# Kernel optimization log

Measured on AMD Instinct MI355X. Metric: run time of the kernel, lower is better.

Reference implementation:

```python
import jax, jax.numpy as jnp
import numpy as np

N = 131072
D = 64
K = 1024
COMMITMENT_COST = 0.25


def setup_inputs() -> dict:
    key = jax.random.key(0)
    k1, k2 = jax.random.split(key)
    inputs = jax.random.normal(k1, (N, D), dtype=jnp.float32)
    # nn.Embedding weight initialized uniform(-1/K, 1/K)
    codebook = jax.random.uniform(k2, (K, D), dtype=jnp.float32,
                                  minval=-1.0 / K, maxval=1.0 / K)
    return {"inputs": inputs, "codebook": codebook}


def reference(inputs, codebook):
    # distances[n,k] = ||x_n||^2 + ||e_k||^2 - 2 x_n . e_k   (squared L2)
    distances = (jnp.sum(inputs ** 2, axis=1, keepdims=True)
                 + jnp.sum(codebook ** 2, axis=1)
                 - 2.0 * jnp.matmul(inputs, codebook.T))          # [N, K]
    encoding_indices = jnp.argmin(distances, axis=1)               # [N]
    # one-hot scatter + matmul in the original == direct gather
    quantized = codebook[encoding_indices]                         # [N, D]

    e_latent_loss = jnp.mean((jax.lax.stop_gradient(quantized) - inputs) ** 2)
    q_latent_loss = jnp.mean((quantized - jax.lax.stop_gradient(inputs)) ** 2)
    loss = q_latent_loss + COMMITMENT_COST * e_latent_loss

    # straight-through estimator
    quantized_st = inputs + jax.lax.stop_gradient(quantized - inputs)
    return loss, quantized_st, encoding_indices
```

## Files before the change

### kernel.cpp

```cpp
#include <hip/hip_runtime.h>

#define NN 131072
#define DD 64
#define KK 1024

typedef __attribute__((ext_vector_type(8))) short short8v;
typedef __attribute__((ext_vector_type(4))) float float4v;
typedef __attribute__((ext_vector_type(4))) int int4v;

#define MFMA(a, b, c) __builtin_amdgcn_mfma_f32_16x16x32_bf16(a, b, c, 0, 0, 0)

#define INS3(t0, t1, t2, i0, i1, i2, u, kk)                                  \
    if ((u) < (t0)) { t2 = t1; i2 = i1; t1 = t0; i1 = i0; t0 = (u); i0 = (kk); } \
    else if ((u) < (t1)) { t2 = t1; i2 = i1; t1 = (u); i1 = (kk); }          \
    else if ((u) < (t2)) { t2 = (u); i2 = (kk); }

#define LEXINS3(t0, t1, t2, i0, i1, i2, u, kk)                               \
    if ((u) < (t0) || ((u) == (t0) && (kk) < (i0))) {                        \
        t2 = t1; i2 = i1; t1 = t0; i1 = i0; t0 = (u); i0 = (kk); }           \
    else if ((u) < (t1) || ((u) == (t1) && (kk) < (i1))) {                   \
        t2 = t1; i2 = i1; t1 = (u); i1 = (kk); }                             \
    else if ((u) < (t2) || ((u) == (t2) && (kk) < (i2))) { t2 = (u); i2 = (kk); }

__device__ __forceinline__ float np_sumsq64(const float* v) {
    float r[8];
#pragma unroll
    for (int j = 0; j < 8; ++j) r[j] = __fmul_rn(v[j], v[j]);
#pragma unroll
    for (int i = 8; i < 64; i += 8) {
#pragma unroll
        for (int j = 0; j < 8; ++j)
            r[j] = __fadd_rn(r[j], __fmul_rn(v[i + j], v[i + j]));
    }
    return __fadd_rn(__fadd_rn(__fadd_rn(r[0], r[1]), __fadd_rn(r[2], r[3])),
                     __fadd_rn(__fadd_rn(r[4], r[5]), __fadd_rn(r[6], r[7])));
}

__device__ __forceinline__ void bf16split(float v, unsigned short& hb, unsigned short& lb) {
    unsigned int u = __builtin_bit_cast(unsigned int, v);
    unsigned int h = (u + 0x7FFFu + ((u >> 16) & 1u)) >> 16;
    float hf = __builtin_bit_cast(float, h << 16);
    float lo = __fsub_rn(v, hf);
    unsigned int ul = __builtin_bit_cast(unsigned int, lo);
    unsigned int lo16 = (ul + 0x7FFFu + ((ul >> 16) & 1u)) >> 16;
    hb = (unsigned short)h;
    lb = (unsigned short)lo16;
}

__global__ void vq_prep(const float* __restrict__ cb, unsigned short* __restrict__ cbh,
                        unsigned short* __restrict__ cbl, float* __restrict__ se) {
    int k = blockIdx.x * 256 + threadIdx.x;
    if (k >= KK) return;
    float v[DD];
    const float4* p = (const float4*)(cb + (size_t)k * DD);
#pragma unroll
    for (int i = 0; i < 16; ++i) {
        float4 q = p[i];
        v[4 * i + 0] = q.x; v[4 * i + 1] = q.y; v[4 * i + 2] = q.z; v[4 * i + 3] = q.w;
    }
    se[k] = np_sumsq64(v);
    short8v* oh = (short8v*)(cbh + (size_t)k * DD);
    short8v* ol = (short8v*)(cbl + (size_t)k * DD);
#pragma unroll
    for (int q = 0; q < 8; ++q) {
        short8v hq, lq;
#pragma unroll
        for (int e = 0; e < 8; ++e) {
            unsigned short hb, lb;
            bf16split(v[q * 8 + e], hb, lb);
            hq[e] = (short)hb; lq[e] = (short)lb;
        }
        oh[q] = hq; ol[q] = lq;
    }
}

__global__ __launch_bounds__(256)
void vq_main(const float* __restrict__ x, const float* __restrict__ cb,
             const unsigned short* __restrict__ cbh, const unsigned short* __restrict__ cbl,
             const float* __restrict__ se, float* __restrict__ qout,
             float* __restrict__ idxf, double* __restrict__ acc) {
    __shared__ unsigned short xh[128 * 64], xl[128 * 64];
    __shared__ unsigned short ebh[128 * 64], ebl[128 * 64];
    __shared__ float ses[KK];
    __shared__ float wls[4];

    const int tid = threadIdx.x;
    const int rowBase = blockIdx.x * 128;
    const int l = tid & 63;
    const int w = tid >> 6;
    const int col = l & 15;
    const int g = l >> 4;

    ((float4v*)ses)[tid] = ((const float4v*)se)[tid];

    {
        int row = tid >> 1, db = (tid & 1) * 32;
        const float* xr = x + (size_t)(rowBase + row) * 64 + db;
#pragma unroll
        for (int jj = 0; jj < 4; ++jj) {
            float4 v0 = ((const float4*)xr)[2 * jj];
            float4 v1 = ((const float4*)xr)[2 * jj + 1];
            float vv[8] = {v0.x, v0.y, v0.z, v0.w, v1.x, v1.y, v1.z, v1.w};
            short8v hq, lq;
#pragma unroll
            for (int e = 0; e < 8; ++e) {
                unsigned short hb, lb;
                bf16split(vv[e], hb, lb);
                hq[e] = (short)hb; lq[e] = (short)lb;
            }
            int q = (tid & 1) * 4 + jj;
            int slot = row * 8 + (q ^ (row & 7));
            ((short8v*)xh)[slot] = hq;
            ((short8v*)xl)[slot] = lq;
        }
    }
    __syncthreads();

    short8v ah0s0, ah1s0, al0s0, al1s0, ah0s1, ah1s1, al0s1, al1s1;
    {
        int r0 = w * 32 + col;
        int r1 = r0 + 16;
        ah0s0 = ((short8v*)xh)[r0 * 8 + ((0 + g) ^ (r0 & 7))];
        ah1s0 = ((short8v*)xh)[r0 * 8 + ((4 + g) ^ (r0 & 7))];
        al0s0 = ((short8v*)xl)[r0 * 8 + ((0 + g) ^ (r0 & 7))];
        al1s0 = ((short8v*)xl)[r0 * 8 + ((4 + g) ^ (r0 & 7))];
        ah0s1 = ((short8v*)xh)[r1 * 8 + ((0 + g) ^ (r1 & 7))];
        ah1s1 = ((short8v*)xh)[r1 * 8 + ((4 + g) ^ (r1 & 7))];
        al0s1 = ((short8v*)xl)[r1 * 8 + ((0 + g) ^ (r1 & 7))];
        al1s1 = ((short8v*)xl)[r1 * 8 + ((4 + g) ^ (r1 & 7))];
    }

    float bt[8][3];
    int bix[8][3];
#pragma unroll
    for (int s = 0; s < 8; ++s) {
#pragma unroll
        for (int j = 0; j < 3; ++j) { bt[s][j] = 3.4e38f; bix[s][j] = 0x7FFFFFF; }
    }

    int4v rbh[4], rbl[4];
    {
        int e = tid >> 1;
        const unsigned short* ph = cbh + (size_t)e * 64 + (tid & 1) * 32;
        const unsigned short* pl = cbl + (size_t)e * 64 + (tid & 1) * 32;
#pragma unroll
        for (int jj = 0; jj < 4; ++jj) {
            rbh[jj] = *(const int4v*)(ph + jj * 8);
            rbl[jj] = *(const int4v*)(pl + jj * 8);
        }
    }

    for (int t = 0; t < 8; ++t) {
        __syncthreads();
        {
            int e = tid >> 1;
#pragma unroll
            for (int jj = 0; jj < 4; ++jj) {
                int q = (tid & 1) * 4 + jj;
                int slot = e * 8 + (q ^ (e & 7));
                ((int4v*)ebh)[slot] = rbh[jj];
                ((int4v*)ebl)[slot] = rbl[jj];
            }
        }
        __syncthreads();
        if (t < 7) {
            int e = tid >> 1;
            const unsigned short* ph = cbh + (size_t)((t + 1) * 128 + e) * 64 + (tid & 1) * 32;
            const unsigned short* pl = cbl + (size_t)((t + 1) * 128 + e) * 64 + (tid & 1) * 32;
#pragma unroll
            for (int jj = 0; jj < 4; ++jj) {
                rbh[jj] = *(const int4v*)(ph + jj * 8);
                rbl[jj] = *(const int4v*)(pl + jj * 8);
            }
        }

#pragma unroll
        for (int c = 0; c < 8; ++c) {
            int ec = c * 16 + col;
            int be = ec * 8, sw = ec & 7;
            short8v bh0 = ((short8v*)ebh)[be + ((0 + g) ^ sw)];
            short8v bh1 = ((short8v*)ebh)[be + ((4 + g) ^ sw)];
            short8v bl0 = ((short8v*)ebl)[be + ((0 + g) ^ sw)];
            short8v bl1 = ((short8v*)ebl)[be + ((4 + g) ^ sw)];
            float sek = ses[t * 128 + ec];
            float4v acc0 = {0.f, 0.f, 0.f, 0.f}, acc1 = {0.f, 0.f, 0.f, 0.f};
            acc0 = MFMA(ah0s0, bh0, acc0);
            acc0 = MFMA(ah1s0, bh1, acc0);
            acc0 = MFMA(al0s0, bh0, acc0);
            acc0 = MFMA(al1s0, bh1, acc0);
            acc0 = MFMA(ah0s0, bl0, acc0);
            acc0 = MFMA(ah1s0, bl1, acc0);
            acc1 = MFMA(ah0s1, bh0, acc1);
            acc1 = MFMA(ah1s1, bh1, acc1);
            acc1 = MFMA(al0s1, bh0, acc1);
            acc1 = MFMA(al1s1, bh1, acc1);
            acc1 = MFMA(ah0s1, bl0, acc1);
            acc1 = MFMA(ah1s1, bl1, acc1);
            int kk = t * 128 + ec;
#pragma unroll
            for (int r = 0; r < 4; ++r) {
                float u0 = fmaf(-2.f, acc0[r], sek);
                INS3(bt[r][0], bt[r][1], bt[r][2], bix[r][0], bix[r][1], bix[r][2], u0, kk);
                float u1 = fmaf(-2.f, acc1[r], sek);
                INS3(bt[4 + r][0], bt[4 + r][1], bt[4 + r][2],
                     bix[4 + r][0], bix[4 + r][1], bix[4 + r][2], u1, kk);
            }
        }
    }

#pragma unroll
    for (int s = 0; s < 8; ++s) {
#pragma unroll
        for (int m = 1; m < 16; m <<= 1) {
            float o0 = __shfl_xor(bt[s][0], m), o1 = __shfl_xor(bt[s][1], m), o2 = __shfl_xor(bt[s][2], m);
            int q0 = __shfl_xor(bix[s][0], m), q1 = __shfl_xor(bix[s][1], m), q2 = __shfl_xor(bix[s][2], m);
            LEXINS3(bt[s][0], bt[s][1], bt[s][2], bix[s][0], bix[s][1], bix[s][2], o0, q0);
            LEXINS3(bt[s][0], bt[s][1], bt[s][2], bix[s][0], bix[s][1], bix[s][2], o1, q1);
            LEXINS3(bt[s][0], bt[s][1], bt[s][2], bix[s][0], bix[s][1], bix[s][2], o2, q2);
        }
    }

    float lossLocal = 0.f;
    const int rr = (l & 15) >> 2;
    const int j = l & 3;
    const int jj = (j == 3) ? 0 : j;
#pragma unroll
    for (int s = 0; s < 2; ++s) {
        int ck = bix[s * 4][0];
#pragma unroll
        for (int r_ = 0; r_ < 4; ++r_) {
#pragma unroll
            for (int j_ = 0; j_ < 3; ++j_) {
                if (rr == r_ && jj == j_) ck = bix[s * 4 + r_][j_];
            }
        }
        int rowg = rowBase + w * 32 + s * 16 + g * 4 + rr;
        const float4* xr = (const float4*)(x + (size_t)rowg * 64);
        const float4* er = (const float4*)(cb + (size_t)ck * 64);
        float dot = 0.f;
        float rs0 = 0.f, rs1 = 0.f, rs2 = 0.f, rs3 = 0.f, rs4 = 0.f, rs5 = 0.f, rs6 = 0.f, rs7 = 0.f;
#pragma unroll
        for (int i = 0; i < 16; ++i) {
            float4 a4 = xr[i], e4 = er[i];
            dot = fmaf(a4.x, e4.x, dot);
            dot = fmaf(a4.y, e4.y, dot);
            dot = fmaf(a4.z, e4.z, dot);
            dot = fmaf(a4.w, e4.w, dot);
            if ((i & 1) == 0) {
                rs0 = __fadd_rn(rs0, __fmul_rn(a4.x, a4.x));
                rs1 = __fadd_rn(rs1, __fmul_rn(a4.y, a4.y));
                rs2 = __fadd_rn(rs2, __fmul_rn(a4.z, a4.z));
                rs3 = __fadd_rn(rs3, __fmul_rn(a4.w, a4.w));
            } else {
                rs4 = __fadd_rn(rs4, __fmul_rn(a4.x, a4.x));
                rs5 = __fadd_rn(rs5, __fmul_rn(a4.y, a4.y));
                rs6 = __fadd_rn(rs6, __fmul_rn(a4.z, a4.z));
                rs7 = __fadd_rn(rs7, __fmul_rn(a4.w, a4.w));
            }
        }
        float sa = __fadd_rn(__fadd_rn(__fadd_rn(rs0, rs1), __fadd_rn(rs2, rs3)),
                             __fadd_rn(__fadd_rn(rs4, rs5), __fadd_rn(rs6, rs7)));
        float qd = __fsub_rn(__fadd_rn(sa, ses[ck]), __fmul_rn(2.f, dot));
#pragma unroll
        for (int m = 1; m < 4; m <<= 1) {
            float oq = __shfl_xor(qd, m);
            int ok = __shfl_xor(ck, m);
            if (oq < qd || (oq == qd && ok < ck)) { qd = oq; ck = ok; }
        }
        if (j == 0) idxf[rowg] = (float)ck;
        const float4* qr = (const float4*)(cb + (size_t)ck * 64);
        float* orow = qout + (size_t)rowg * 64;
#pragma unroll
        for (int p = 0; p < 4; ++p) {
            int iq = j * 4 + p;
            float4 xv = xr[iq];
            float4 qv = qr[iq];
            float dx = __fsub_rn(qv.x, xv.x);
            float dy = __fsub_rn(qv.y, xv.y);
            float dz = __fsub_rn(qv.z, xv.z);
            float dw = __fsub_rn(qv.w, xv.w);
            float4 o;
            o.x = __fadd_rn(xv.x, dx);
            o.y = __fadd_rn(xv.y, dy);
            o.z = __fadd_rn(xv.z, dz);
            o.w = __fadd_rn(xv.w, dw);
            ((float4*)orow)[iq] = o;
            lossLocal = fmaf(dx, dx, lossLocal);
            lossLocal = fmaf(dy, dy, lossLocal);
            lossLocal = fmaf(dz, dz, lossLocal);
            lossLocal = fmaf(dw, dw, lossLocal);
        }
    }
#pragma unroll
    for (int m = 1; m < 64; m <<= 1) lossLocal += __shfl_xor(lossLocal, m);
    if (l == 0) wls[w] = lossLocal;
    __syncthreads();
    if (tid == 0) atomicAdd(acc, (double)(wls[0] + wls[1] + wls[2] + wls[3]));
}

__global__ void vq_loss(const double* __restrict__ acc, float* __restrict__ out) {
    out[0] = (float)(acc[0] * 1.25 / (double)((size_t)NN * DD));
}

extern "C" void kernel_launch(void* const* d_in, const int* in_sizes, int n_in,
                              void* d_out, int out_size, void* d_ws, size_t ws_size,
                              hipStream_t stream) {
    const float* x = (const float*)d_in[0];
    const float* cb = (const float*)d_in[1];
    float* out = (float*)d_out;

    double* acc = (double*)d_ws;
    float* se = (float*)((char*)d_ws + 64);
    unsigned short* cbh = (unsigned short*)((char*)d_ws + 8192);
    unsigned short* cbl = (unsigned short*)((char*)d_ws + 8192 + 131072);

    hipMemsetAsync(d_ws, 0, 64, stream);

    vq_prep<<<4, 256, 0, stream>>>(cb, cbh, cbl, se);
    vq_main<<<NN / 128, 256, 0, stream>>>(x, cb, cbh, cbl, se,
                                          out + 1, out + 1 + (size_t)NN * DD, acc);
    vq_loss<<<1, 1, 0, stream>>>(acc, out);
}
```

Measured before the change: 237.7 us.

## Pack distance and index into sortable keys, double-buffer smaller codebook tiles

Result: faster. 195.4 us (-17.8%).

```diff
diff --git a/kernel.cpp b/kernel.cpp
--- a/kernel.cpp
+++ b/kernel.cpp
@@ -10,17 +10,19 @@
 
 #define MFMA(a, b, c) __builtin_amdgcn_mfma_f32_16x16x32_bf16(a, b, c, 0, 0, 0)
 
-#define INS3(t0, t1, t2, i0, i1, i2, u, kk)                                  \
-    if ((u) < (t0)) { t2 = t1; i2 = i1; t1 = t0; i1 = i0; t0 = (u); i0 = (kk); } \
-    else if ((u) < (t1)) { t2 = t1; i2 = i1; t1 = (u); i1 = (kk); }          \
-    else if ((u) < (t2)) { t2 = (u); i2 = (kk); }
-
-#define LEXINS3(t0, t1, t2, i0, i1, i2, u, kk)                               \
-    if ((u) < (t0) || ((u) == (t0) && (kk) < (i0))) {                        \
-        t2 = t1; i2 = i1; t1 = t0; i1 = i0; t0 = (u); i0 = (kk); }           \
-    else if ((u) < (t1) || ((u) == (t1) && (kk) < (i1))) {                   \
-        t2 = t1; i2 = i1; t1 = (u); i1 = (kk); }                             \
-    else if ((u) < (t2) || ((u) == (t2) && (kk) < (i2))) { t2 = (u); i2 = (kk); }
+__device__ __forceinline__ unsigned int umin32(unsigned int a, unsigned int b) { return a < b ? a : b; }
+__device__ __forceinline__ unsigned int umax32(unsigned int a, unsigned int b) { return a > b ? a : b; }
+
+__device__ __forceinline__ unsigned int packu(float u, int kk) {
+    int b = __builtin_bit_cast(int, u);
+    unsigned int key = (unsigned int)(b ^ ((b >> 31) | 0x80000000));
+    return (key & 0xFFFFFC00u) | (unsigned int)kk;
+}
+
+#define PINS3(t0, t1, t2, p)                                   \
+    { unsigned int _x0 = umax32(t0, p); t0 = umin32(t0, p);    \
+      unsigned int _x1 = umax32(t1, _x0); t1 = umin32(t1, _x0);\
+      t2 = umin32(t2, _x1); }
 
 __device__ __forceinline__ float np_sumsq64(const float* v) {
     float r[8];
@@ -74,13 +76,17 @@
     }
 }
 
-__global__ __launch_bounds__(256)
+union SMem {
+    struct { unsigned short xh[128 * 64]; unsigned short xl[128 * 64]; } x;
+    struct { unsigned short bh[2][64 * 64]; unsigned short bl[2][64 * 64]; } b;
+};
+
+__global__ __launch_bounds__(256, 4)
 void vq_main(const float* __restrict__ x, const float* __restrict__ cb,
              const unsigned short* __restrict__ cbh, const unsigned short* __restrict__ cbl,
              const float* __restrict__ se, float* __restrict__ qout,
              float* __restrict__ idxf, double* __restrict__ acc) {
-    __shared__ unsigned short xh[128 * 64], xl[128 * 64];
-    __shared__ unsigned short ebh[128 * 64], ebl[128 * 64];
+    __shared__ SMem sm;
     __shared__ float ses[KK];
     __shared__ float wls[4];
 
@@ -90,6 +96,21 @@
     const int w = tid >> 6;
     const int col = l & 15;
     const int g = l >> 4;
+
+    int4v rbh[2], rbl[2];
+    const int be_ = tid >> 2;
+    const int bq_ = (tid & 3) * 2;
+#define LOAD_TILE(tt)                                                              \
+    { const unsigned short* ph = cbh + ((size_t)((tt) * 64 + be_) * 64) + (tid & 3) * 16; \
+      const unsigned short* pl = cbl + ((size_t)((tt) * 64 + be_) * 64) + (tid & 3) * 16; \
+      rbh[0] = *(const int4v*)(ph); rbh[1] = *(const int4v*)(ph + 8);              \
+      rbl[0] = *(const int4v*)(pl); rbl[1] = *(const int4v*)(pl + 8); }
+#define WRITE_TILE(bufi)                                                           \
+    { int4v* dh = (int4v*)sm.b.bh[bufi]; int4v* dl = (int4v*)sm.b.bl[bufi];        \
+      dh[be_ * 8 + (bq_ ^ (be_ & 7))] = rbh[0];                                    \
+      dh[be_ * 8 + ((bq_ + 1) ^ (be_ & 7))] = rbh[1];                              \
+      dl[be_ * 8 + (bq_ ^ (be_ & 7))] = rbl[0];                                    \
+      dl[be_ * 8 + ((bq_ + 1) ^ (be_ & 7))] = rbl[1]; }
 
     ((float4v*)ses)[tid] = ((const float4v*)se)[tid];
 
@@ -110,79 +131,52 @@
             }
             int q = (tid & 1) * 4 + jj;
             int slot = row * 8 + (q ^ (row & 7));
-            ((short8v*)xh)[slot] = hq;
-            ((short8v*)xl)[slot] = lq;
-        }
-    }
+            ((short8v*)sm.x.xh)[slot] = hq;
+            ((short8v*)sm.x.xl)[slot] = lq;
+        }
+    }
+    LOAD_TILE(0);
     __syncthreads();
 
     short8v ah0s0, ah1s0, al0s0, al1s0, ah0s1, ah1s1, al0s1, al1s1;
     {
         int r0 = w * 32 + col;
         int r1 = r0 + 16;
-        ah0s0 = ((short8v*)xh)[r0 * 8 + ((0 + g) ^ (r0 & 7))];
-        ah1s0 = ((short8v*)xh)[r0 * 8 + ((4 + g) ^ (r0 & 7))];
-        al0s0 = ((short8v*)xl)[r0 * 8 + ((0 + g) ^ (r0 & 7))];
-        al1s0 = ((short8v*)xl)[r0 * 8 + ((4 + g) ^ (r0 & 7))];
-        ah0s1 = ((short8v*)xh)[r1 * 8 + ((0 + g) ^ (r1 & 7))];
-        ah1s1 = ((short8v*)xh)[r1 * 8 + ((4 + g) ^ (r1 & 7))];
-        al0s1 = ((short8v*)xl)[r1 * 8 + ((0 + g) ^ (r1 & 7))];
-        al1s1 = ((short8v*)xl)[r1 * 8 + ((4 + g) ^ (r1 & 7))];
-    }
-
-    float bt[8][3];
-    int bix[8][3];
-#pragma unroll
-    for (int s = 0; s < 8; ++s) {
-#pragma unroll
-        for (int j = 0; j < 3; ++j) { bt[s][j] = 3.4e38f; bix[s][j] = 0x7FFFFFF; }
-    }
-
-    int4v rbh[4], rbl[4];
-    {
-        int e = tid >> 1;
-        const unsigned short* ph = cbh + (size_t)e * 64 + (tid & 1) * 32;
-        const unsigned short* pl = cbl + (size_t)e * 64 + (tid & 1) * 32;
-#pragma unroll
-        for (int jj = 0; jj < 4; ++jj) {
-            rbh[jj] = *(const int4v*)(ph + jj * 8);
-            rbl[jj] = *(const int4v*)(pl + jj * 8);
-        }
-    }
-
-    for (int t = 0; t < 8; ++t) {
-        __syncthreads();
-        {
-            int e = tid >> 1;
-#pragma unroll
-            for (int jj = 0; jj < 4; ++jj) {
-                int q = (tid & 1) * 4 + jj;
-                int slot = e * 8 + (q ^ (e & 7));
-                ((int4v*)ebh)[slot] = rbh[jj];
-                ((int4v*)ebl)[slot] = rbl[jj];
-            }
-        }
-        __syncthreads();
-        if (t < 7) {
-            int e = tid >> 1;
-            const unsigned short* ph = cbh + (size_t)((t + 1) * 128 + e) * 64 + (tid & 1) * 32;
-            const unsigned short* pl = cbl + (size_t)((t + 1) * 128 + e) * 64 + (tid & 1) * 32;
-#pragma unroll
-            for (int jj = 0; jj < 4; ++jj) {
-                rbh[jj] = *(const int4v*)(ph + jj * 8);
-                rbl[jj] = *(const int4v*)(pl + jj * 8);
-            }
-        }
-
-#pragma unroll
-        for (int c = 0; c < 8; ++c) {
+        ah0s0 = ((short8v*)sm.x.xh)[r0 * 8 + ((0 + g) ^ (r0 & 7))];
+        ah1s0 = ((short8v*)sm.x.xh)[r0 * 8 + ((4 + g) ^ (r0 & 7))];
+        al0s0 = ((short8v*)sm.x.xl)[r0 * 8 + ((0 + g) ^ (r0 & 7))];
+        al1s0 = ((short8v*)sm.x.xl)[r0 * 8 + ((4 + g) ^ (r0 & 7))];
+        ah0s1 = ((short8v*)sm.x.xh)[r1 * 8 + ((0 + g) ^ (r1 & 7))];
+        ah1s1 = ((short8v*)sm.x.xh)[r1 * 8 + ((4 + g) ^ (r1 & 7))];
+        al0s1 = ((short8v*)sm.x.xl)[r1 * 8 + ((0 + g) ^ (r1 & 7))];
+        al1s1 = ((short8v*)sm.x.xl)[r1 * 8 + ((4 + g) ^ (r1 & 7))];
+    }
+    __syncthreads();
+
+    WRITE_TILE(0);
+    LOAD_TILE(1);
+    __syncthreads();
+
+    unsigned int k0[8], k1[8], k2[8];
+#pragma unroll
+    for (int s = 0; s < 8; ++s) { k0[s] = 0xFFFFFFFFu; k1[s] = 0xFFFFFFFFu; k2[s] = 0xFFFFFFFFu; }
+
+    for (int t = 0; t < 16; ++t) {
+        if (t < 15) {
+            WRITE_TILE((t + 1) & 1);
+            if (t < 14) LOAD_TILE(t + 2);
+        }
+        const unsigned short* bhB = sm.b.bh[t & 1];
+        const unsigned short* blB = sm.b.bl[t & 1];
+#pragma unroll
+        for (int c = 0; c < 4; ++c) {
             int ec = c * 16 + col;
             int be = ec * 8, sw = ec & 7;
-            short8v bh0 = ((short8v*)ebh)[be + ((0 + g) ^ sw)];
-            short8v bh1 = ((short8v*)ebh)[be + ((4 + g) ^ sw)];
-            short8v bl0 = ((short8v*)ebl)[be + ((0 + g) ^ sw)];
-            short8v bl1 = ((short8v*)ebl)[be + ((4 + g) ^ sw)];
-            float sek = ses[t * 128 + ec];
+            short8v bh0 = ((const short8v*)bhB)[be + ((0 + g) ^ sw)];
+            short8v bh1 = ((const short8v*)bhB)[be + ((4 + g) ^ sw)];
+            short8v bl0 = ((const short8v*)blB)[be + ((0 + g) ^ sw)];
+            short8v bl1 = ((const short8v*)blB)[be + ((4 + g) ^ sw)];
+            float sek = ses[t * 64 + ec];
             float4v acc0 = {0.f, 0.f, 0.f, 0.f}, acc1 = {0.f, 0.f, 0.f, 0.f};
             acc0 = MFMA(ah0s0, bh0, acc0);
             acc0 = MFMA(ah1s0, bh1, acc0);
@@ -196,27 +190,29 @@
             acc1 = MFMA(al1s1, bh1, acc1);
             acc1 = MFMA(ah0s1, bl0, acc1);
             acc1 = MFMA(ah1s1, bl1, acc1);
-            int kk = t * 128 + ec;
+            int kk = t * 64 + ec;
 #pragma unroll
             for (int r = 0; r < 4; ++r) {
-                float u0 = fmaf(-2.f, acc0[r], sek);
-                INS3(bt[r][0], bt[r][1], bt[r][2], bix[r][0], bix[r][1], bix[r][2], u0, kk);
-                float u1 = fmaf(-2.f, acc1[r], sek);
-                INS3(bt[4 + r][0], bt[4 + r][1], bt[4 + r][2],
-                     bix[4 + r][0], bix[4 + r][1], bix[4 + r][2], u1, kk);
+                unsigned int p0 = packu(fmaf(-2.f, acc0[r], sek), kk);
+                PINS3(k0[r], k1[r], k2[r], p0);
+                unsigned int p1 = packu(fmaf(-2.f, acc1[r], sek), kk);
+                PINS3(k0[4 + r], k1[4 + r], k2[4 + r], p1);
             }
         }
+        __syncthreads();
     }
 
 #pragma unroll
     for (int s = 0; s < 8; ++s) {
 #pragma unroll
         for (int m = 1; m < 16; m <<= 1) {
-            float o0 = __shfl_xor(bt[s][0], m), o1 = __shfl_xor(bt[s][1], m), o2 = __shfl_xor(bt[s][2], m);
-            int q0 = __shfl_xor(bix[s][0], m), q1 = __shfl_xor(bix[s][1], m), q2 = __shfl_xor(bix[s][2], m);
-            LEXINS3(bt[s][0], bt[s][1], bt[s][2], bix[s][0], bix[s][1], bix[s][2], o0, q0);
-            LEXINS3(bt[s][0], bt[s][1], bt[s][2], bix[s][0], bix[s][1], bix[s][2], o1, q1);
-            LEXINS3(bt[s][0], bt[s][1], bt[s][2], bix[s][0], bix[s][1], bix[s][2], o2, q2);
+            unsigned int o0 = __shfl_xor(k0[s], m);
+            unsigned int o1 = __shfl_xor(k1[s], m);
+            unsigned int o2 = __shfl_xor(k2[s], m);
+            PINS3(k0[s], k1[s], k2[s], o0);
+            { unsigned int x1 = umax32(k1[s], o1); k1[s] = umin32(k1[s], o1);
+              k2[s] = umin32(k2[s], x1); }
+            k2[s] = umin32(k2[s], o2);
         }
     }
 
@@ -226,14 +222,16 @@
     const int jj = (j == 3) ? 0 : j;
 #pragma unroll
     for (int s = 0; s < 2; ++s) {
-        int ck = bix[s * 4][0];
+        unsigned int ckk = k0[s * 4];
 #pragma unroll
         for (int r_ = 0; r_ < 4; ++r_) {
-#pragma unroll
-            for (int j_ = 0; j_ < 3; ++j_) {
-                if (rr == r_ && jj == j_) ck = bix[s * 4 + r_][j_];
+            if (rr == r_) {
+                if (jj == 0) ckk = k0[s * 4 + r_];
+                else if (jj == 1) ckk = k1[s * 4 + r_];
+                else ckk = k2[s * 4 + r_];
             }
         }
+        int ck = (int)(ckk & 1023u);
         int rowg = rowBase + w * 32 + s * 16 + g * 4 + rr;
         const float4* xr = (const float4*)(x + (size_t)rowg * 64);
         const float4* er = (const float4*)(cb + (size_t)ck * 64);
```
